# Kernel tuning notes

Hardware: AMD Instinct MI355X
Metric: run time of the kernel (lower is better)

## Reference

```python
import jax, jax.numpy as jnp
import numpy as np

NUM_NODES = 50000
NUM_RELATIONS = 16
HIDDEN = 128
NUM_LAYERS = 3
NUM_EDGES = 1600000


def setup_inputs() -> dict:
    key = jax.random.key(0)
    ks = jax.random.split(key, 6)
    edge_index = jax.random.randint(ks[0], (2, NUM_EDGES), 0, NUM_NODES, dtype=jnp.int64)
    edge_type = jax.random.randint(ks[1], (NUM_EDGES,), 0, NUM_RELATIONS, dtype=jnp.int64)
    scale = 1.0 / np.sqrt(HIDDEN)
    node_init = jax.random.normal(ks[2], (NUM_NODES, HIDDEN), dtype=jnp.float32) * scale
    W = jax.random.normal(ks[3], (NUM_LAYERS, NUM_RELATIONS, HIDDEN, HIDDEN), dtype=jnp.float32) * scale
    root = jax.random.normal(ks[4], (NUM_LAYERS, HIDDEN, HIDDEN), dtype=jnp.float32) * scale
    bias = jnp.zeros((NUM_LAYERS, HIDDEN), dtype=jnp.float32)
    return {"edge_index": edge_index, "edge_type": edge_type,
            "node_init": node_init, "W": W, "root": root, "bias": bias}


def _fast_rgcn_layer(x, src, tgt, edge_type, W_r, root_r, bias_r):
    # FastRGCNConv with aggr='mean': mean of messages per (target node, relation),
    # message = x_src @ W[relation]. By linearity, aggregate normalized x_src per
    # (node, relation) first, then apply relation weights with a single einsum.
    N, d = x.shape
    R = W_r.shape[0]
    seg = tgt * R + edge_type                       # combined (node, relation) segment id
    msg = x[src]                                    # [E, d] irregular gather
    agg = jax.ops.segment_sum(msg, seg, num_segments=N * R).reshape(N, R, d)
    cnt = jax.ops.segment_sum(jnp.ones_like(edge_type, dtype=x.dtype), seg,
                              num_segments=N * R).reshape(N, R, 1)
    agg = agg / jnp.clip(cnt, 1.0, None)            # per-(node,relation) mean
    out = jnp.einsum('nrd,rdo->no', agg, W_r)       # relation-specific transform
    out = out + x @ root_r + bias_r                 # root/self connection + bias
    return out


def reference(edge_index, edge_type, node_init, W, root, bias):
    src, tgt = edge_index[0], edge_index[1]
    x = node_init
    for i in range(NUM_LAYERS):
        x = _fast_rgcn_layer(x, src, tgt, edge_type, W[i], root[i], bias[i])
        if i < NUM_LAYERS - 1:
            x = jax.nn.relu(x)  # dropout omitted (eval mode)
    return x
```

## Files before the change

### kernel.cpp

```cpp
#include <hip/hip_runtime.h>
#include <hip/hip_bf16.h>

#define N_NODES   50000
#define N_REL     16
#define HID       128
#define N_EDGES   1600000
#define N_TILES   3125
#define N_BINS    800000
#define N_RUNS    50000
#define N_SCANBLK 49
#define N_MBLK    1563
#define PAYLOAD_CAP 2400064
#define BS_LAYER  278528
#define AG_STRIDE 136

typedef unsigned short ushort_t;
typedef __attribute__((ext_vector_type(8))) short short8;
typedef __attribute__((ext_vector_type(4))) float f32x4;

union BF2U { __hip_bfloat162 h; unsigned u; };

__device__ __forceinline__ unsigned pack_bf16_2(float x, float y) {
  BF2U c; c.h = __float22bfloat162_rn(make_float2(x, y));
  return c.u;
}

__device__ __forceinline__ void lds_barrier() {
  asm volatile("s_waitcnt lgkmcnt(0)\n\ts_barrier" ::: "memory");
}


__global__ __launch_bounds__(256) void k_hist(const int* __restrict__ ei,
                                              const int* __restrict__ et,
                                              int* __restrict__ cnt,
                                              int* __restrict__ rank) {
  int e = blockIdx.x * 256 + threadIdx.x;
  int tgt = ei[N_EDGES + e];
  int r   = et[e];
  int key = ((tgt >> 4) << 8) | (r << 4) | (tgt & 15);
  rank[e] = atomicAdd(&cnt[key], 1);
}

__global__ __launch_bounds__(1024) void k_runpad_btot(const int* __restrict__ cnt,
                                                      int* __restrict__ run_start,
                                                      int* __restrict__ totals) {
  __shared__ int s[1024];
  int t = threadIdx.x, blk = blockIdx.x;
  int r = blk * 1024 + t;
  int v = 0;
  if (r < N_RUNS) {
    const int4* c4 = (const int4*)(cnt + r * 16);
    int sum = 0;
#pragma unroll
    for (int j = 0; j < 4; ++j) { int4 w = c4[j]; sum += w.x + w.y + w.z + w.w; }
    v = (sum + 15) & ~15;
    run_start[r] = v;
  }
  s[t] = v; __syncthreads();
  for (int ofs = 512; ofs > 0; ofs >>= 1) {
    if (t < ofs) s[t] += s[t + ofs];
    __syncthreads();
  }
  if (t == 0) totals[blk] = s[0];
}

__global__ __launch_bounds__(1024) void k_scan_totals(int* totals, int* endp, int nblk) {
  __shared__ int s[1024];
  int t = threadIdx.x;
  int v = (t < nblk) ? totals[t] : 0;
  s[t] = v; __syncthreads();
  for (int ofs = 1; ofs < 1024; ofs <<= 1) {
    int x = (t >= ofs) ? s[t - ofs] : 0;
    __syncthreads();
    s[t] += x;
    __syncthreads();
  }
  if (t < nblk) totals[t] = s[t] - v;
  if (t == nblk - 1) *endp = s[t];
}

__global__ __launch_bounds__(1024) void k_scan_fineoff(int* __restrict__ run_start,
                                                       const int* __restrict__ totals,
                                                       const int* __restrict__ cnt,
                                                       int* __restrict__ fine_start,
                                                       unsigned* __restrict__ payload) {
  __shared__ int s[1024];
  int t = threadIdx.x, blk = blockIdx.x;
  int r = blk * 1024 + t;
  int v = (r < N_RUNS) ? run_start[r] : 0;
  s[t] = v; __syncthreads();
  for (int ofs = 1; ofs < 1024; ofs <<= 1) {
    int x = (t >= ofs) ? s[t - ofs] : 0;
    __syncthreads();
    s[t] += x;
    __syncthreads();
  }
  if (r < N_RUNS) {
    int base = totals[blk] + s[t] - v;
    run_start[r] = base;
    int pfx = 0;
#pragma unroll 4
    for (int i = 0; i < 16; ++i) {
      fine_start[r * 16 + i] = base + pfx;
      pfx += cnt[r * 16 + i];
    }
    const unsigned dummy = ((unsigned)N_NODES << 16) | (1u << 4) | 15u;
    for (int j = base + pfx; j < base + v; ++j) payload[j] = dummy;
  }
}

__global__ __launch_bounds__(256) void k_sort(const int* __restrict__ ei,
                                              const int* __restrict__ et,
                                              const int* __restrict__ cnt,
                                              const int* __restrict__ fine_start,
                                              const int* __restrict__ rank,
                                              unsigned* __restrict__ payload) {
  int e = blockIdx.x * 256 + threadIdx.x;
  int src = ei[e];
  int tgt = ei[N_EDGES + e];
  int r   = et[e];
  int key = ((tgt >> 4) << 8) | (r << 4) | (tgt & 15);
  int c = cnt[key]; c = c > 4095 ? 4095 : c;
  int pos = fine_start[key] + rank[e];
  payload[pos] = ((unsigned)src << 16) | ((unsigned)c << 4) | (unsigned)(tgt & 15);
}

__global__ __launch_bounds__(256) void k_bt(const float* __restrict__ W,
                                            const float* __restrict__ root,
                                            ushort_t* __restrict__ Bs) {
  int idx = blockIdx.x * 256 + threadIdx.x;
  int lane = idx & 63;
  int fl   = idx >> 6;
  int frag = fl % 544;
  int l    = fl / 544;
  int cb = frag & 7, kk = (frag >> 3) & 3, r = frag >> 5;
  int col = cb * 16 + (lane & 15);
  int d0  = kk * 32 + (lane >> 4) * 8;
  const float* srcp = (r < 16)
      ? W + ((size_t)(l * N_REL + r) * HID + d0) * HID + col
      : root + ((size_t)l * HID + d0) * HID + col;
  ushort_t out[8];
#pragma unroll
  for (int j = 0; j < 8; ++j) {
    union { __hip_bfloat16 h; ushort_t u; } c;
    c.h = __float2bfloat16(srcp[(size_t)j * HID]);
    out[j] = c.u;
  }
  *(short8*)(Bs + ((size_t)fl << 9) + lane * 8) = *(short8*)out;
}

__global__ __launch_bounds__(256) void k_xh(const float* __restrict__ xin,
                                            ushort_t* __restrict__ xh_a,
                                            ushort_t* __restrict__ xh_b) {
  int i = blockIdx.x * 256 + threadIdx.x;
  float4 v = ((const float4*)xin)[i];
  uint2 u;
  u.x = pack_bf16_2(v.x, v.y);
  u.y = pack_bf16_2(v.z, v.w);
  ((uint2*)xh_a)[i] = u;
  if (blockIdx.x == 0 && threadIdx.x < 64) {
    uint2 z = {0u, 0u};
    ushort_t* dst = (threadIdx.x < 32) ? xh_a : xh_b;
    int k = threadIdx.x & 31;
    *(uint2*)(dst + (size_t)N_NODES * HID + k * 4) = z;
  }
}


__global__ __launch_bounds__(256, 3) void k_main(const ushort_t* __restrict__ xh,
                                                 ushort_t* __restrict__ xh_out,
                                                 float* __restrict__ fout,
                                                 const ushort_t* __restrict__ Bs,
                                                 const float* __restrict__ bias,
                                                 const int* __restrict__ run_start,
                                                 const unsigned* __restrict__ payload,
                                                 int write_f32) {
  __shared__ alignas(16) ushort_t agg[2][2][32][AG_STRIDE];

  const int tile0 = blockIdx.x * 2;
  const int tid   = threadIdx.x;
  const int wave  = tid >> 6;
  const int lane  = tid & 63;
  const int m16   = lane & 15;
  const int q     = lane >> 4;
  const unsigned* xh32 = (const unsigned*)xh;

  if (wave < 2) {
    const int p = wave;
    int ebv = 0;
    {
      int s8 = lane >> 2, t2 = (lane >> 1) & 1, h = lane & 1;
      int tt = tile0 + t2;
      int idx = (tt < N_TILES) ? (tt * 16 + s8 * 2 + p + h) : N_RUNS;
      if (lane < 32) ebv = run_start[idx];
    }

#define ISSUE16(DST, PV, JB)                                                  \
    _Pragma("unroll")                                                         \
    for (int k1 = 0; k1 < 16; ++k1) {                                         \
      unsigned spq = (unsigned)__builtin_amdgcn_readlane(PV, (JB) + k1);      \
      DST[k1] = xh32[(spq >> 16) * 64 + lane];                                \
    }

#define FLUSHM(TB, BUF)                                                       \
    if (mcur >= 0) {                                                          \
      float sc = __builtin_amdgcn_rcpf((float)scnt);                          \
      *(unsigned*)&agg[BUF][p][(TB) + mcur][lane * 2] =                       \
          pack_bf16_2(a0 * sc, a1 * sc);                                      \
    }

#define CONSUME1(SPK, XV, TB, BUF)                                            \
    {                                                                         \
      int mk = (int)((SPK) & 15u);                                            \
      if (mk != mcur) {                                                       \
        FLUSHM(TB, BUF);                                                      \
        mcur = mk; scnt = (int)(((SPK) >> 4) & 4095u);                        \
        a0 = 0.f; a1 = 0.f;                                                   \
      }                                                                       \
      a0 += __uint_as_float((XV) << 16);                                      \
      a1 += __uint_as_float((XV) & 0xffff0000u);                              \
    }

#define CONS16(PV, JB, SLOT, TB, BUF)                                         \
    _Pragma("unroll")                                                         \
    for (int k2 = 0; k2 < 16; ++k2) {                                         \
      unsigned spk = (unsigned)__builtin_amdgcn_readlane(PV, (JB) + k2);      \
      CONSUME1(spk, SLOT[k2], TB, BUF);                                       \
    }

#define RUNX(PV, E0, E1, CNT, B0, B1, TB)                                     \
    {                                                                         \
      int mcur = -1, scnt = 1;                                                \
      float a0 = 0.f, a1 = 0.f;                                               \
      if ((CNT) > 0) {                                                        \
        CONS16(PV, 0, B0, TB, buf);                                           \
        if ((CNT) > 16) {                                                     \
          CONS16(PV, 16, B1, TB, buf);                                        \
          if ((CNT) > 32) {                                                   \
            CONS16(PV, 32, xqE, TB, buf);                                     \
            if ((CNT) > 48) {                                                 \
              ISSUE16(xqE, PV, 48);                                           \
              CONS16(PV, 48, xqE, TB, buf);                                   \
            }                                                                 \
          }                                                                   \
        }                                                                     \
        for (int c0 = (E0) + 64; c0 < (E1); c0 += 16) {        \
          int pvx = (int)payload[c0 + lane];                                  \
          ISSUE16(xqE, pvx, 0);                                               \
          CONS16(pvx, 0, xqE, TB, buf);                                       \
        }                                                                     \
        FLUSHM(TB, buf);                                                      \
      }                                                                       \
    }

    unsigned xqA[16], xqB[16], xqC[16], xqD[16], xqE[16];

    int e00 = __builtin_amdgcn_readlane(ebv, 0);
    int e01 = __builtin_amdgcn_readlane(ebv, 1);
    int e10 = __builtin_amdgcn_readlane(ebv, 2);
    int e11 = __builtin_amdgcn_readlane(ebv, 3);
    int pv0 = (int)payload[e00 + lane];
    int pv1 = (int)payload[e10 + lane];
    ISSUE16(xqA, pv0, 0);
    ISSUE16(xqC, pv1, 0);
    __builtin_amdgcn_sched_barrier(0);

    for (int s = 0; s < 8; ++s) {
      const int buf = s & 1;
      int cnt0 = e01 - e00, cnt1 = e11 - e10;

      if (cnt0 > 16) ISSUE16(xqB, pv0, 16);
      if (cnt1 > 16) ISSUE16(xqD, pv1, 16);
      if (cnt0 > 32) ISSUE16(xqE, pv0, 32);

      int f00 = e00, f01 = e01, f10 = e10, f11 = e11;
      int pvn0 = pv0, pvn1 = pv1;
      if (s < 7) {
        f00 = __builtin_amdgcn_readlane(ebv, (s + 1) * 4 + 0);
        f01 = __builtin_amdgcn_readlane(ebv, (s + 1) * 4 + 1);
        f10 = __builtin_amdgcn_readlane(ebv, (s + 1) * 4 + 2);
        f11 = __builtin_amdgcn_readlane(ebv, (s + 1) * 4 + 3);
        pvn0 = (int)payload[f00 + lane];
        pvn1 = (int)payload[f10 + lane];
      }
      __builtin_amdgcn_sched_barrier(0);

      {
        short8 z = {0, 0, 0, 0, 0, 0, 0, 0};
#pragma unroll
        for (int i = 0; i < 8; ++i)
          *(short8*)&agg[buf][p][i * 4 + q][m16 * 8] = z;
      }

      RUNX(pv0, e00, e01, cnt0, xqA, xqB, 0);
      if (cnt1 > 32) ISSUE16(xqE, pv1, 32);
      __builtin_amdgcn_sched_barrier(0);
      RUNX(pv1, e10, e11, cnt1, xqC, xqD, 16);

      if (s < 7) {
        e00 = f00; e01 = f01; e10 = f10; e11 = f11;
        pv0 = pvn0; pv1 = pvn1;
        ISSUE16(xqA, pv0, 0);
        ISSUE16(xqC, pv1, 0);
      }
      __builtin_amdgcn_sched_barrier(0);
      lds_barrier();
    }
#undef RUNX
#undef CONS16
#undef CONSUME1
#undef FLUSHM
#undef ISSUE16
    return;
  }

  const int c = wave - 2;
  f32x4 acc[2][4];
#pragma unroll
  for (int t = 0; t < 2; ++t)
#pragma unroll
    for (int i = 0; i < 4; ++i) acc[t][i] = (f32x4){0.f, 0.f, 0.f, 0.f};

  for (int s = 0; s < 8; ++s) {
    lds_barrier();
#pragma unroll
    for (int rp = 0; rp < 2; ++rp) {
      int rel = s * 2 + rp;
      short8 Bf[4][4];
#pragma unroll
      for (int kk = 0; kk < 4; ++kk)
#pragma unroll
        for (int i = 0; i < 4; ++i)
          Bf[kk][i] = *(const short8*)(Bs +
              ((size_t)((rel * 4 + kk) * 8 + (c * 4 + i)) << 9) + lane * 8);
#pragma unroll
      for (int kk = 0; kk < 4; ++kk) {
        short8 A0 = *(const short8*)&agg[s & 1][rp][m16][kk * 32 + q * 8];
        short8 A1 = *(const short8*)&agg[s & 1][rp][16 + m16][kk * 32 + q * 8];
#pragma unroll
        for (int i = 0; i < 4; ++i) {
          acc[0][i] = __builtin_amdgcn_mfma_f32_16x16x32_bf16(A0, Bf[kk][i], acc[0][i], 0, 0, 0);
          acc[1][i] = __builtin_amdgcn_mfma_f32_16x16x32_bf16(A1, Bf[kk][i], acc[1][i], 0, 0, 0);
        }
      }
    }
  }

  {
    short8 Bf[4][4];
#pragma unroll
    for (int kk = 0; kk < 4; ++kk)
#pragma unroll
      for (int i = 0; i < 4; ++i)
        Bf[kk][i] = *(const short8*)(Bs +
            ((size_t)((16 * 4 + kk) * 8 + (c * 4 + i)) << 9) + lane * 8);
    int r0 = tile0 * 16 + m16;      if (r0 > N_NODES) r0 = N_NODES;
    int r1 = tile0 * 16 + 16 + m16; if (r1 > N_NODES) r1 = N_NODES;
#pragma unroll
    for (int kk = 0; kk < 4; ++kk) {
      short8 A0 = *(const short8*)(xh + (size_t)r0 * HID + kk * 32 + q * 8);
      short8 A1 = *(const short8*)(xh + (size_t)r1 * HID + kk * 32 + q * 8);
#pragma unroll
      for (int i = 0; i < 4; ++i) {
        acc[0][i] = __builtin_amdgcn_mfma_f32_16x16x32_bf16(A0, Bf[kk][i], acc[0][i], 0, 0, 0);
        acc[1][i] = __builtin_amdgcn_mfma_f32_16x16x32_bf16(A1, Bf[kk][i], acc[1][i], 0, 0, 0);
      }
    }
  }

  float bvv[4];
#pragma unroll
  for (int i = 0; i < 4; ++i) bvv[i] = bias[(c * 4 + i) * 16 + m16];
  int rbase = tile0 * 16 + q * 4;
#pragma unroll
  for (int t = 0; t < 2; ++t)
#pragma unroll
    for (int rg = 0; rg < 4; ++rg) {
      int row = rbase + t * 16 + rg;
      if (row < N_NODES) {
#pragma unroll
        for (int i = 0; i < 4; ++i) {
          float v = acc[t][i][rg] + bvv[i];
          int col = (c * 4 + i) * 16 + m16;
          if (write_f32) {
            fout[(size_t)row * HID + col] = v;
          } else {
            v = fmaxf(v, 0.f);
            union { __hip_bfloat16 h; ushort_t u; } cv;
            cv.h = __float2bfloat16(v);
            xh_out[(size_t)row * HID + col] = cv.u;
          }
        }
      }
    }
}


extern "C" void kernel_launch(void* const* d_in, const int* in_sizes, int n_in,
                              void* d_out, int out_size, void* d_ws, size_t ws_size,
                              hipStream_t stream) {
  const int*   ei        = (const int*)d_in[0];
  const int*   et        = (const int*)d_in[1];
  const float* node_init = (const float*)d_in[2];
  const float* W         = (const float*)d_in[3];
  const float* root      = (const float*)d_in[4];
  const float* bias      = (const float*)d_in[5];
  float* outp = (float*)d_out;

  char* ws = (char*)d_ws;
  size_t o = 0;
  auto carve = [&](size_t bytes) { char* p = ws + o; o = (o + bytes + 255) & ~(size_t)255; return p; };
  ushort_t* xh_a       = (ushort_t*)carve((size_t)(N_NODES + 1) * HID * 2);
  ushort_t* xh_b       = (ushort_t*)carve((size_t)(N_NODES + 1) * HID * 2);
  unsigned* payload    = (unsigned*)carve((size_t)PAYLOAD_CAP * 4);
  int*      cnt        = (int*)     carve((size_t)N_BINS * 4);
  int*      fine_start = (int*)     carve((size_t)N_BINS * 4);
  int*      rank       = (int*)     carve((size_t)N_EDGES * 4);
  int*      run_start  = (int*)     carve((size_t)(N_RUNS + 1) * 4);
  int*      totals     = (int*)     carve((size_t)N_SCANBLK * 4);
  ushort_t* Bs         = (ushort_t*)carve((size_t)3 * BS_LAYER * 2);
  (void)ws_size; (void)n_in; (void)in_sizes; (void)out_size;

  hipMemsetAsync(cnt, 0, (size_t)N_BINS * 4, stream);
  hipLaunchKernelGGL(k_hist,         dim3(N_EDGES / 256), dim3(256), 0, stream, ei, et, cnt, rank);
  hipLaunchKernelGGL(k_runpad_btot,  dim3(N_SCANBLK), dim3(1024), 0, stream, cnt, run_start, totals);
  hipLaunchKernelGGL(k_scan_totals,  dim3(1), dim3(1024), 0, stream, totals, run_start + N_RUNS, N_SCANBLK);
  hipLaunchKernelGGL(k_scan_fineoff, dim3(N_SCANBLK), dim3(1024), 0, stream, run_start, totals, cnt, fine_start, payload);
  hipLaunchKernelGGL(k_sort,         dim3(N_EDGES / 256), dim3(256), 0, stream, ei, et, cnt, fine_start, rank, payload);
  hipLaunchKernelGGL(k_bt,           dim3(3 * 544 * 64 / 256), dim3(256), 0, stream, W, root, Bs);
  hipLaunchKernelGGL(k_xh,           dim3(N_NODES * HID / 4 / 256), dim3(256), 0, stream, node_init, xh_a, xh_b);

  hipLaunchKernelGGL(k_main, dim3(N_MBLK), dim3(256), 0, stream,
                     xh_a, xh_b, (float*)nullptr,
                     Bs + (size_t)0 * BS_LAYER, bias + 0 * HID, run_start, payload, 0);
  hipLaunchKernelGGL(k_main, dim3(N_MBLK), dim3(256), 0, stream,
                     xh_b, xh_a, (float*)nullptr,
                     Bs + (size_t)1 * BS_LAYER, bias + 1 * HID, run_start, payload, 0);
  hipLaunchKernelGGL(k_main, dim3(N_MBLK), dim3(256), 0, stream,
                     xh_a, (ushort_t*)nullptr, outp,
                     Bs + (size_t)2 * BS_LAYER, bias + 2 * HID, run_start, payload, 1);
}
```

Baseline: 611.9 us.

## Double wave count per block, splitting gather per tile and MFMA columns

The main fused layer kernel now launches 512 threads (8 waves) per block instead of 256. Four gather waves each handle one (tile, relation-parity) pair instead of two waves each covering two tiles. Four MFMA waves each compute 32 output columns instead of two waves covering 64. The aim is more memory-level parallelism for the irregular gather and more resident waves to hide latency. In exchange the per-wave prefetch depth shrinks (fewer register buffers, no explicit sched barriers), and the new launch bounds constrain register use, which could cause spills.

```diff
diff --git a/kernel.cpp b/kernel.cpp
--- a/kernel.cpp
+++ b/kernel.cpp
@@ -167,7 +167,7 @@
 }
 
 
-__global__ __launch_bounds__(256, 3) void k_main(const ushort_t* __restrict__ xh,
+__global__ __launch_bounds__(512, 8) void k_main(const ushort_t* __restrict__ xh,
                                                  ushort_t* __restrict__ xh_out,
                                                  float* __restrict__ fout,
                                                  const ushort_t* __restrict__ Bs,
@@ -185,14 +185,17 @@
   const int q     = lane >> 4;
   const unsigned* xh32 = (const unsigned*)xh;
 
-  if (wave < 2) {
-    const int p = wave;
+  if (wave < 4) {
+    const int p_rel  = wave & 1;
+    const int p_tile = wave >> 1;
+    const int rowb   = p_tile * 16;
+
     int ebv = 0;
     {
-      int s8 = lane >> 2, t2 = (lane >> 1) & 1, h = lane & 1;
-      int tt = tile0 + t2;
-      int idx = (tt < N_TILES) ? (tt * 16 + s8 * 2 + p + h) : N_RUNS;
-      if (lane < 32) ebv = run_start[idx];
+      int tt = tile0 + p_tile;
+      int idx = (tt < N_TILES) ? (tt * 16 + (lane >> 1) * 2 + p_rel + (lane & 1))
+                               : N_RUNS;
+      if (lane < 16) ebv = run_start[idx];
     }
 
 #define ISSUE16(DST, PV, JB)                                                  \
@@ -202,18 +205,18 @@
       DST[k1] = xh32[(spq >> 16) * 64 + lane];                                \
     }
 
-#define FLUSHM(TB, BUF)                                                       \
+#define FLUSHM(BUF)                                                           \
     if (mcur >= 0) {                                                          \
       float sc = __builtin_amdgcn_rcpf((float)scnt);                          \
-      *(unsigned*)&agg[BUF][p][(TB) + mcur][lane * 2] =                       \
+      *(unsigned*)&agg[BUF][p_rel][rowb + mcur][lane * 2] =                   \
           pack_bf16_2(a0 * sc, a1 * sc);                                      \
     }
 
-#define CONSUME1(SPK, XV, TB, BUF)                                            \
+#define CONSUME1(SPK, XV, BUF)                                                \
     {                                                                         \
       int mk = (int)((SPK) & 15u);                                            \
       if (mk != mcur) {                                                       \
-        FLUSHM(TB, BUF);                                                      \
+        FLUSHM(BUF);                                                          \
         mcur = mk; scnt = (int)(((SPK) >> 4) & 4095u);                        \
         a0 = 0.f; a1 = 0.f;                                                   \
       }                                                                       \
@@ -221,92 +224,71 @@
       a1 += __uint_as_float((XV) & 0xffff0000u);                              \
     }
 
-#define CONS16(PV, JB, SLOT, TB, BUF)                                         \
+#define CONS16(PV, JB, SLOT, BUF)                                             \
     _Pragma("unroll")                                                         \
     for (int k2 = 0; k2 < 16; ++k2) {                                         \
       unsigned spk = (unsigned)__builtin_amdgcn_readlane(PV, (JB) + k2);      \
-      CONSUME1(spk, SLOT[k2], TB, BUF);                                       \
-    }
-
-#define RUNX(PV, E0, E1, CNT, B0, B1, TB)                                     \
-    {                                                                         \
-      int mcur = -1, scnt = 1;                                                \
-      float a0 = 0.f, a1 = 0.f;                                               \
-      if ((CNT) > 0) {                                                        \
-        CONS16(PV, 0, B0, TB, buf);                                           \
-        if ((CNT) > 16) {                                                     \
-          CONS16(PV, 16, B1, TB, buf);                                        \
-          if ((CNT) > 32) {                                                   \
-            CONS16(PV, 32, xqE, TB, buf);                                     \
-            if ((CNT) > 48) {                                                 \
-              ISSUE16(xqE, PV, 48);                                           \
-              CONS16(PV, 48, xqE, TB, buf);                                   \
-            }                                                                 \
-          }                                                                   \
-        }                                                                     \
-        for (int c0 = (E0) + 64; c0 < (E1); c0 += 16) {        \
-          int pvx = (int)payload[c0 + lane];                                  \
-          ISSUE16(xqE, pvx, 0);                                               \
-          CONS16(pvx, 0, xqE, TB, buf);                                       \
-        }                                                                     \
-        FLUSHM(TB, buf);                                                      \
-      }                                                                       \
-    }
-
-    unsigned xqA[16], xqB[16], xqC[16], xqD[16], xqE[16];
-
-    int e00 = __builtin_amdgcn_readlane(ebv, 0);
-    int e01 = __builtin_amdgcn_readlane(ebv, 1);
-    int e10 = __builtin_amdgcn_readlane(ebv, 2);
-    int e11 = __builtin_amdgcn_readlane(ebv, 3);
-    int pv0 = (int)payload[e00 + lane];
-    int pv1 = (int)payload[e10 + lane];
-    ISSUE16(xqA, pv0, 0);
-    ISSUE16(xqC, pv1, 0);
-    __builtin_amdgcn_sched_barrier(0);
+      CONSUME1(spk, SLOT[k2], BUF);                                           \
+    }
+
+    unsigned xqA[16], xqB[16], xqE[16];
+
+    int e0 = __builtin_amdgcn_readlane(ebv, 0);
+    int e1 = __builtin_amdgcn_readlane(ebv, 1);
+    int pv = (int)payload[e0 + lane];
+    ISSUE16(xqA, pv, 0);
 
     for (int s = 0; s < 8; ++s) {
       const int buf = s & 1;
-      int cnt0 = e01 - e00, cnt1 = e11 - e10;
-
-      if (cnt0 > 16) ISSUE16(xqB, pv0, 16);
-      if (cnt1 > 16) ISSUE16(xqD, pv1, 16);
-      if (cnt0 > 32) ISSUE16(xqE, pv0, 32);
-
-      int f00 = e00, f01 = e01, f10 = e10, f11 = e11;
-      int pvn0 = pv0, pvn1 = pv1;
+      int cnt = e1 - e0;
+
+      if (cnt > 16) ISSUE16(xqB, pv, 16);
+      if (cnt > 32) ISSUE16(xqE, pv, 32);
+
+      int f0 = e0, f1 = e1, pvn = pv;
       if (s < 7) {
-        f00 = __builtin_amdgcn_readlane(ebv, (s + 1) * 4 + 0);
-        f01 = __builtin_amdgcn_readlane(ebv, (s + 1) * 4 + 1);
-        f10 = __builtin_amdgcn_readlane(ebv, (s + 1) * 4 + 2);
-        f11 = __builtin_amdgcn_readlane(ebv, (s + 1) * 4 + 3);
-        pvn0 = (int)payload[f00 + lane];
-        pvn1 = (int)payload[f10 + lane];
-      }
-      __builtin_amdgcn_sched_barrier(0);
+        f0 = __builtin_amdgcn_readlane(ebv, (s + 1) * 2);
+        f1 = __builtin_amdgcn_readlane(ebv, (s + 1) * 2 + 1);
+        pvn = (int)payload[f0 + lane];
+      }
 
       {
         short8 z = {0, 0, 0, 0, 0, 0, 0, 0};
 #pragma unroll
-        for (int i = 0; i < 8; ++i)
-          *(short8*)&agg[buf][p][i * 4 + q][m16 * 8] = z;
-      }
-
-      RUNX(pv0, e00, e01, cnt0, xqA, xqB, 0);
-      if (cnt1 > 32) ISSUE16(xqE, pv1, 32);
-      __builtin_amdgcn_sched_barrier(0);
-      RUNX(pv1, e10, e11, cnt1, xqC, xqD, 16);
+        for (int i = 0; i < 4; ++i)
+          *(short8*)&agg[buf][p_rel][rowb + i * 4 + q][m16 * 8] = z;
+      }
+
+      {
+        int mcur = -1, scnt = 1;
+        float a0 = 0.f, a1 = 0.f;
+        if (cnt > 0) {
+          CONS16(pv, 0, xqA, buf);
+          if (cnt > 16) {
+            CONS16(pv, 16, xqB, buf);
+            if (cnt > 32) {
+              CONS16(pv, 32, xqE, buf);
+              if (cnt > 48) {
+                ISSUE16(xqB, pv, 48);
+                CONS16(pv, 48, xqB, buf);
+              }
+            }
+          }
+          for (int c0 = e0 + 64; c0 < e1; c0 += 16) {
+            int pvx = (int)payload[c0 + lane];
+            ISSUE16(xqE, pvx, 0);
+            CONS16(pvx, 0, xqE, buf);
+          }
+          FLUSHM(buf);
+        }
+      }
 
       if (s < 7) {
-        e00 = f00; e01 = f01; e10 = f10; e11 = f11;
-        pv0 = pvn0; pv1 = pvn1;
-        ISSUE16(xqA, pv0, 0);
-        ISSUE16(xqC, pv1, 0);
-      }
-      __builtin_amdgcn_sched_barrier(0);
+        e0 = f0; e1 = f1; pv = pvn;
+        ISSUE16(xqA, pv, 0);
+      }
       lds_barrier();
     }
-#undef RUNX
 #undef CONS16
 #undef CONSUME1
 #undef FLUSHM
@@ -314,31 +296,31 @@
     return;
   }
 
-  const int c = wave - 2;
-  f32x4 acc[2][4];
+  const int cw = wave - 4;
+  f32x4 acc[2][2];
 #pragma unroll
   for (int t = 0; t < 2; ++t)
 #pragma unroll
-    for (int i = 0; i < 4; ++i) acc[t][i] = (f32x4){0.f, 0.f, 0.f, 0.f};
+    for (int i = 0; i < 2; ++i) acc[t][i] = (f32x4){0.f, 0.f, 0.f, 0.f};
 
   for (int s = 0; s < 8; ++s) {
     lds_barrier();
 #pragma unroll
     for (int rp = 0; rp < 2; ++rp) {
       int rel = s * 2 + rp;
-      short8 Bf[4][4];
+      short8 Bf[4][2];
 #pragma unroll
       for (int kk = 0; kk < 4; ++kk)
 #pragma unroll
-        for (int i = 0; i < 4; ++i)
+        for (int i = 0; i < 2; ++i)
           Bf[kk][i] = *(const short8*)(Bs +
-              ((size_t)((rel * 4 + kk) * 8 + (c * 4 + i)) << 9) + lane * 8);
+              ((size_t)((rel * 4 + kk) * 8 + (cw * 2 + i)) << 9) + lane * 8);
 #pragma unroll
       for (int kk = 0; kk < 4; ++kk) {
         short8 A0 = *(const short8*)&agg[s & 1][rp][m16][kk * 32 + q * 8];
         short8 A1 = *(const short8*)&agg[s & 1][rp][16 + m16][kk * 32 + q * 8];
 #pragma unroll
-        for (int i = 0; i < 4; ++i) {
+        for (int i = 0; i < 2; ++i) {
           acc[0][i] = __builtin_amdgcn_mfma_f32_16x16x32_bf16(A0, Bf[kk][i], acc[0][i], 0, 0, 0);
           acc[1][i] = __builtin_amdgcn_mfma_f32_16x16x32_bf16(A1, Bf[kk][i], acc[1][i], 0, 0, 0);
         }
@@ -347,13 +329,13 @@
   }
 
   {
-    short8 Bf[4][4];
+    short8 Bf[4][2];
 #pragma unroll
     for (int kk = 0; kk < 4; ++kk)
 #pragma unroll
-      for (int i = 0; i < 4; ++i)
+      for (int i = 0; i < 2; ++i)
         Bf[kk][i] = *(const short8*)(Bs +
-            ((size_t)((16 * 4 + kk) * 8 + (c * 4 + i)) << 9) + lane * 8);
+            ((size_t)((16 * 4 + kk) * 8 + (cw * 2 + i)) << 9) + lane * 8);
     int r0 = tile0 * 16 + m16;      if (r0 > N_NODES) r0 = N_NODES;
     int r1 = tile0 * 16 + 16 + m16; if (r1 > N_NODES) r1 = N_NODES;
 #pragma unroll
@@ -361,16 +343,16 @@
       short8 A0 = *(const short8*)(xh + (size_t)r0 * HID + kk * 32 + q * 8);
       short8 A1 = *(const short8*)(xh + (size_t)r1 * HID + kk * 32 + q * 8);
 #pragma unroll
-      for (int i = 0; i < 4; ++i) {
+      for (int i = 0; i < 2; ++i) {
         acc[0][i] = __builtin_amdgcn_mfma_f32_16x16x32_bf16(A0, Bf[kk][i], acc[0][i], 0, 0, 0);
         acc[1][i] = __builtin_amdgcn_mfma_f32_16x16x32_bf16(A1, Bf[kk][i], acc[1][i], 0, 0, 0);
       }
     }
   }
 
-  float bvv[4];
-#pragma unroll
-  for (int i = 0; i < 4; ++i) bvv[i] = bias[(c * 4 + i) * 16 + m16];
+  float bvv[2];
+#pragma unroll
+  for (int i = 0; i < 2; ++i) bvv[i] = bias[cw * 32 + i * 16 + m16];
   int rbase = tile0 * 16 + q * 4;
 #pragma unroll
   for (int t = 0; t < 2; ++t)
@@ -379,9 +361,9 @@
       int row = rbase + t * 16 + rg;
       if (row < N_NODES) {
 #pragma unroll
-        for (int i = 0; i < 4; ++i) {
+        for (int i = 0; i < 2; ++i) {
           float v = acc[t][i][rg] + bvv[i];
-          int col = (c * 4 + i) * 16 + m16;
+          int col = cw * 32 + i * 16 + m16;
           if (write_f32) {
             fout[(size_t)row * HID + col] = v;
           } else {
@@ -430,13 +412,13 @@
   hipLaunchKernelGGL(k_bt,           dim3(3 * 544 * 64 / 256), dim3(256), 0, stream, W, root, Bs);
   hipLaunchKernelGGL(k_xh,           dim3(N_NODES * HID / 4 / 256), dim3(256), 0, stream, node_init, xh_a, xh_b);
 
-  hipLaunchKernelGGL(k_main, dim3(N_MBLK), dim3(256), 0, stream,
+  hipLaunchKernelGGL(k_main, dim3(N_MBLK), dim3(512), 0, stream,
                      xh_a, xh_b, (float*)nullptr,
                      Bs + (size_t)0 * BS_LAYER, bias + 0 * HID, run_start, payload, 0);
-  hipLaunchKernelGGL(k_main, dim3(N_MBLK), dim3(256), 0, stream,
+  hipLaunchKernelGGL(k_main, dim3(N_MBLK), dim3(512), 0, stream,
                      xh_b, xh_a, (float*)nullptr,
                      Bs + (size_t)1 * BS_LAYER, bias + 1 * HID, run_start, payload, 0);
-  hipLaunchKernelGGL(k_main, dim3(N_MBLK), dim3(256), 0, stream,
+  hipLaunchKernelGGL(k_main, dim3(N_MBLK), dim3(512), 0, stream,
                      xh_a, (ushort_t*)nullptr, outp,
                      Bs + (size_t)2 * BS_LAYER, bias + 2 * HID, run_start, payload, 1);
 }
```

New measurement: 509.0 us. -16.8%, faster.
